# Optimization experiments

Hardware: AMD Instinct MI355X
Metric: run time of the kernel (lower is better)

Reference implementation:

```python
import jax, jax.numpy as jnp
import numpy as np

IN_FEA = 128
OUT_FEA = 128
ALPHA = 0.2  # LeakyReLU negative slope
NEG_INF = -1.0e12


def setup_inputs() -> dict:
    key = jax.random.key(0)
    k1, k2, k3, k4 = jax.random.split(key, 4)
    b, n = 8, 2048
    inp = jax.random.normal(k1, (b, n, IN_FEA), dtype=jnp.float32)
    adj = jax.random.randint(k2, (b, n, n), 0, 2, dtype=jnp.int32)
    # xavier_uniform with gain=1.414
    def xavier(k, shape, gain=1.414):
        fan_in, fan_out = shape[0], shape[1]
        limit = gain * np.sqrt(6.0 / (fan_in + fan_out))
        return jax.random.uniform(k, shape, jnp.float32, -limit, limit)
    W = xavier(k3, (IN_FEA, OUT_FEA))
    a = xavier(k4, (2 * OUT_FEA, 1))
    return {"inp": inp, "adj": adj, "W": W, "a": a}


def reference(inp, adj, W, a):
    # h: [b, n, d]
    h = jnp.matmul(inp, W)
    # Original builds [b, n*n, 2d] via repeat/view; equivalently split a into
    # a1 (applied to h_j, the 'chunks' half) and a2 (applied to h_i).
    d = h.shape[-1]
    a1 = a[:d, 0]   # [d]
    a2 = a[d:, 0]   # [d]
    f1 = jnp.einsum('bnd,d->bn', h, a1)  # contributes per-column (j)
    f2 = jnp.einsum('bnd,d->bn', h, a2)  # contributes per-row (i)
    e = jax.nn.leaky_relu(f2[:, :, None] + f1[:, None, :], negative_slope=ALPHA)  # [b, n, n]
    logits = jnp.where(adj > 0, e, NEG_INF)
    attention = jax.nn.softmax(logits, axis=-1)
    out_h = jnp.matmul(attention, h)
    out_h = jax.nn.elu(out_h) + h  # concat=True branch
    return out_h
```

## Files before the change

### kernel.cpp

```cpp
#include <hip/hip_runtime.h>
#include <hip/hip_bf16.h>

typedef __bf16 bf16x8 __attribute__((ext_vector_type(8)));
typedef __bf16 bf16x4 __attribute__((ext_vector_type(4)));
typedef float  f32x4  __attribute__((ext_vector_type(4)));

#define LRELU_ALPHA 0.2f
#define LOG2E 1.44269504088896340736f

__device__ __forceinline__ float lrelu(float x) { return fmaxf(x, LRELU_ALPHA * x); }
__device__ __forceinline__ float fexp2(float x) { return exp2f(x); }

__device__ __forceinline__ void wg_barrier() {
    asm volatile("s_waitcnt lgkmcnt(0)" ::: "memory");
    __builtin_amdgcn_s_barrier();
    asm volatile("" ::: "memory");
}

__global__ __launch_bounds__(128) void gat_prep(
    const float* __restrict__ inp, const float* __restrict__ W,
    const float* __restrict__ a,
    float* __restrict__ h, float* __restrict__ f1, float* __restrict__ f2)
{
    const int r0 = blockIdx.x << 3;
    const int d  = threadIdx.x;
    __shared__ float sIn[8][128];
    __shared__ float sRed[8][4];
    #pragma unroll
    for (int r = 0; r < 8; ++r)
        sIn[r][d] = inp[(size_t)(r0 + r) * 128 + d];
    __syncthreads();

    float acc[8] = {0.f,0.f,0.f,0.f,0.f,0.f,0.f,0.f};
    #pragma unroll 4
    for (int k = 0; k < 128; ++k) {
        float wv = W[k * 128 + d];
        #pragma unroll
        for (int r = 0; r < 8; ++r) acc[r] += sIn[r][k] * wv;
    }

    const float a1 = a[d], a2 = a[128 + d];
    const int wv = d >> 6;
    #pragma unroll
    for (int r = 0; r < 8; ++r) {
        h[(size_t)(r0 + r) * 128 + d] = acc[r];
        float t1 = acc[r] * a1;
        float t2 = acc[r] * a2;
        #pragma unroll
        for (int m = 1; m < 64; m <<= 1) {
            t1 += __shfl_xor(t1, m);
            t2 += __shfl_xor(t2, m);
        }
        if ((d & 63) == 0) { sRed[r][wv] = t1; sRed[r][2 + wv] = t2; }
    }
    __syncthreads();
    if (d < 8) {
        f1[r0 + d] = (sRed[d][0] + sRed[d][1]) * LOG2E;
        f2[r0 + d] = (sRed[d][2] + sRed[d][3]) * LOG2E;
    }
}

__global__ __launch_bounds__(256) void gat_f1max(
    const float* __restrict__ f1, float* __restrict__ f1max)
{
    const int b = blockIdx.x;
    const int t = threadIdx.x;
    float m = -1e30f;
    for (int j = t; j < 2048; j += 256) m = fmaxf(m, f1[b * 2048 + j]);
    #pragma unroll
    for (int k = 1; k < 64; k <<= 1) m = fmaxf(m, __shfl_xor(m, k));
    __shared__ float sm[4];
    if ((t & 63) == 0) sm[t >> 6] = m;
    __syncthreads();
    if (t == 0) f1max[b] = fmaxf(fmaxf(sm[0], sm[1]), fmaxf(sm[2], sm[3]));
}

__global__ __launch_bounds__(256) void gat_transpose(
    const float* __restrict__ h, __bf16* __restrict__ hT)
{
    __shared__ __bf16 tile[64][72];
    const int tid = threadIdx.x;
    const int bidx = blockIdx.x;
    const int b  = bidx >> 6;
    const int tI = bidx & 63;
    const int n0 = (tI >> 1) << 6;
    const int d0 = (tI & 1) << 6;
    #pragma unroll
    for (int pass = 0; pass < 2; ++pass) {
        int row = (tid >> 3) + (pass << 5);
        int c   = (tid & 7) << 3;
        const float* src = h + (size_t)(b * 2048 + n0 + row) * 128 + d0 + c;
        float4 v0 = *(const float4*)src;
        float4 v1 = *(const float4*)(src + 4);
        __bf16* tp = &tile[row][c];
        tp[0]=(__bf16)v0.x; tp[1]=(__bf16)v0.y; tp[2]=(__bf16)v0.z; tp[3]=(__bf16)v0.w;
        tp[4]=(__bf16)v1.x; tp[5]=(__bf16)v1.y; tp[6]=(__bf16)v1.z; tp[7]=(__bf16)v1.w;
    }
    __syncthreads();
    #pragma unroll
    for (int pass = 0; pass < 2; ++pass) {
        int dd = (tid >> 3) + (pass << 5);
        int nn = (tid & 7) << 3;
        union { __bf16 e[8]; bf16x8 v; } u;
        #pragma unroll
        for (int x = 0; x < 8; ++x) u.e[x] = tile[nn + x][dd];
        *(bf16x8*)(hT + ((size_t)(b * 128 + d0 + dd) << 11) + n0 + nn) = u.v;
    }
}

#define SWZH(row, byteoff) ((byteoff) ^ (((row) & 7) << 4))

__global__ __launch_bounds__(512, 4) void gat_attn4(
    const int* __restrict__ adj, const float* __restrict__ h,
    const __bf16* __restrict__ hT, const float* __restrict__ f1g,
    const float* __restrict__ f2g, const float* __restrict__ f1maxg,
    float* __restrict__ out)
{
    const int bid = ((blockIdx.x & 7) << 6) | (blockIdx.x >> 3);
    const int b  = bid >> 6;
    const int i0 = (bid & 63) << 5;
    const int tid = threadIdx.x;

    __shared__ float  f1s[2048];
    __shared__ alignas(16) __bf16 hTs[2][128 * 64];
    __shared__ alignas(16) __bf16 Ps[32 * 64];
    __shared__ float  lsum[32];

    *(float4*)&f1s[tid << 2] = *(const float4*)&f1g[(b << 11) + (tid << 2)];

    const int pi  = tid >> 4;
    const int pj4 = tid & 15;
    const float fm  = f1maxg[b];
    const float f2v = f2g[(b << 11) + i0 + pi];
    const float Mshift = lrelu(f2v + fm) - 1000.0f;
    const int* ajp = adj + (((size_t)(b << 11) + i0 + pi) << 11) + (pj4 << 2);
    __bf16* pw = Ps + (pi << 6) + (SWZH(pi, pj4 << 3) >> 1);

    const int hd0 = tid >> 3;
    const int hjc = (tid & 7) << 3;
    const __bf16* hgp0 = hT + (((size_t)(b << 7) + hd0) << 11) + hjc;
    const __bf16* hgp1 = hT + (((size_t)(b << 7) + hd0 + 64) << 11) + hjc;
    const int hw0 = (hd0 << 6) + (SWZH(hd0, hjc << 1) >> 1);
    const int hw1 = ((hd0 + 64) << 6) + (SWZH(hd0, hjc << 1) >> 1);

    const int w    = tid >> 6;
    const int lane = tid & 63;
    const int il   = lane & 15;
    const int kg   = lane >> 4;
    const int ig   = w & 1;
    const int dq   = w >> 1;
    const int ai   = (ig << 4) + il;
    const int d0r  = (dq << 5) + il;
    const int d1r  = d0r + 16;
    const int aof0 = (ai << 6)  + (SWZH(ai,       kg << 4) >> 1);
    const int aof1 = (ai << 6)  + (SWZH(ai, 64 | (kg << 4)) >> 1);
    const int bof00 = (d0r << 6) + (SWZH(d0r,       kg << 4) >> 1);
    const int bof01 = (d0r << 6) + (SWZH(d0r, 64 | (kg << 4)) >> 1);
    const int bof10 = (d1r << 6) + (SWZH(d1r,       kg << 4) >> 1);
    const int bof11 = (d1r << 6) + (SWZH(d1r, 64 | (kg << 4)) >> 1);

    int4   gA  = *(const int4*)ajp;
    int4   gA2 = *(const int4*)(ajp + 64);
    bf16x8 gH0 = *(const bf16x8*)hgp0;
    bf16x8 gH1 = *(const bf16x8*)hgp1;
    *(bf16x8*)(hTs[0] + hw0) = gH0;
    *(bf16x8*)(hTs[0] + hw1) = gH1;
    gH0 = *(const bf16x8*)(hgp0 + 64);
    gH1 = *(const bf16x8*)(hgp1 + 64);

    f32x4 acc0 = {0.f,0.f,0.f,0.f}, acc1 = {0.f,0.f,0.f,0.f};
    float den = 0.f;

    wg_barrier();

    for (int t = 0; t < 32; ++t) {
        int4 adjv = gA;
        gA  = gA2;
        gA2 = *(const int4*)(ajp + (((t + 2) & 31) << 6));

        __bf16* hb = hTs[(t + 1) & 1];
        *(bf16x8*)(hb + hw0) = gH0;
        *(bf16x8*)(hb + hw1) = gH1;
        gH0 = *(const bf16x8*)(hgp0 + (((t + 2) & 31) << 6));
        gH1 = *(const bf16x8*)(hgp1 + (((t + 2) & 31) << 6));

        float4 fv = *(const float4*)&f1s[(t << 6) + (pj4 << 2)];
        float p0, p1, p2, p3;
        { float x = f2v + fv.x; float e = fmaxf(x, LRELU_ALPHA * x) - Mshift;
          p0 = fexp2(__builtin_fmaf(e, (float)adjv.x, -1000.f)); }
        { float x = f2v + fv.y; float e = fmaxf(x, LRELU_ALPHA * x) - Mshift;
          p1 = fexp2(__builtin_fmaf(e, (float)adjv.y, -1000.f)); }
        { float x = f2v + fv.z; float e = fmaxf(x, LRELU_ALPHA * x) - Mshift;
          p2 = fexp2(__builtin_fmaf(e, (float)adjv.z, -1000.f)); }
        { float x = f2v + fv.w; float e = fmaxf(x, LRELU_ALPHA * x) - Mshift;
          p3 = fexp2(__builtin_fmaf(e, (float)adjv.w, -1000.f)); }
        bf16x4 pb;
        pb[0] = (__bf16)p0; pb[1] = (__bf16)p1;
        pb[2] = (__bf16)p2; pb[3] = (__bf16)p3;
        den += (float)pb[0] + (float)pb[1] + (float)pb[2] + (float)pb[3];
        *(bf16x4*)pw = pb;

        wg_barrier();

        const __bf16* hr = hTs[t & 1];
        bf16x8 A0  = *(const bf16x8*)(Ps + aof0);
        bf16x8 A1  = *(const bf16x8*)(Ps + aof1);
        bf16x8 B00 = *(const bf16x8*)(hr + bof00);
        bf16x8 B01 = *(const bf16x8*)(hr + bof01);
        bf16x8 B10 = *(const bf16x8*)(hr + bof10);
        bf16x8 B11 = *(const bf16x8*)(hr + bof11);
        acc0 = __builtin_amdgcn_mfma_f32_16x16x32_bf16(A0, B00, acc0, 0, 0, 0);
        acc0 = __builtin_amdgcn_mfma_f32_16x16x32_bf16(A1, B01, acc0, 0, 0, 0);
        acc1 = __builtin_amdgcn_mfma_f32_16x16x32_bf16(A0, B10, acc1, 0, 0, 0);
        acc1 = __builtin_amdgcn_mfma_f32_16x16x32_bf16(A1, B11, acc1, 0, 0, 0);

        wg_barrier();
    }

    den += __shfl_xor(den, 1);
    den += __shfl_xor(den, 2);
    den += __shfl_xor(den, 4);
    den += __shfl_xor(den, 8);
    if (pj4 == 0) lsum[pi] = den;
    wg_barrier();

    #pragma unroll
    for (int r = 0; r < 4; ++r) {
        const int   row = (kg << 2) + r;
        const float dn  = lsum[(ig << 4) + row];
        const size_t gbase = (((size_t)(b << 11) + i0 + (ig << 4) + row) << 7)
                             + (dq << 5) + il;
        float v, e;
        v = acc0[r] / dn; e = (v > 0.f) ? v : (__expf(v) - 1.f); out[gbase]      = e + h[gbase];
        v = acc1[r] / dn; e = (v > 0.f) ? v : (__expf(v) - 1.f); out[gbase + 16] = e + h[gbase + 16];
    }
}

extern "C" void kernel_launch(void* const* d_in, const int* in_sizes, int n_in,
                              void* d_out, int out_size, void* d_ws, size_t ws_size,
                              hipStream_t stream)
{
    const float* inp = (const float*)d_in[0];
    const int*   adj = (const int*)d_in[1];
    const float* W   = (const float*)d_in[2];
    const float* a   = (const float*)d_in[3];
    float* out = (float*)d_out;

    char* ws = (char*)d_ws;
    float*  h     = (float*)ws;
    __bf16* hT    = (__bf16*)(ws + 8388608);
    float*  f1    = (float*)(ws + 8388608 + 4194304);
    float*  f2    = (float*)(ws + 8388608 + 4194304 + 65536);
    float*  f1max = (float*)(ws + 8388608 + 4194304 + 131072);

    gat_prep<<<2048, 128, 0, stream>>>(inp, W, a, h, f1, f2);
    gat_f1max<<<8, 256, 0, stream>>>(f1, f1max);
    gat_transpose<<<512, 256, 0, stream>>>(h, hT);
    gat_attn4<<<512, 512, 0, stream>>>(adj, h, hT, f1, f2, f1max, out);
}
```

Before: 61.48 us.

## Pre-pack h into MFMA fragment layout and software-pipeline P computation

The transpose kernel now writes h in bf16, already arranged in the per-lane MFMA B-fragment order. The attention kernel loads B operands straight from global memory into registers and no longer stages them through LDS. The loop is restructured so the probabilities for the next tile are computed while the current tile's MFMAs run, using a double-buffered P tile with one barrier per iteration instead of two. This cuts LDS traffic and synchronisation, but every block now reads the packed h directly from global or L2 memory, and register pressure rises.

```diff
diff --git a/kernel.cpp b/kernel.cpp
--- a/kernel.cpp
+++ b/kernel.cpp
@@ -8,7 +8,6 @@
 #define LRELU_ALPHA 0.2f
 #define LOG2E 1.44269504088896340736f
 
-__device__ __forceinline__ float lrelu(float x) { return fmaxf(x, LRELU_ALPHA * x); }
 __device__ __forceinline__ float fexp2(float x) { return exp2f(x); }
 
 __device__ __forceinline__ void wg_barrier() {
@@ -75,10 +74,10 @@
     if (t == 0) f1max[b] = fmaxf(fmaxf(sm[0], sm[1]), fmaxf(sm[2], sm[3]));
 }
 
-__global__ __launch_bounds__(256) void gat_transpose(
-    const float* __restrict__ h, __bf16* __restrict__ hT)
-{
-    __shared__ __bf16 tile[64][72];
+__global__ __launch_bounds__(256) void gat_pack(
+    const float* __restrict__ h, __bf16* __restrict__ pack)
+{
+    __shared__ __bf16 tile[64][74];
     const int tid = threadIdx.x;
     const int bidx = blockIdx.x;
     const int b  = bidx >> 6;
@@ -97,22 +96,46 @@
         tp[4]=(__bf16)v1.x; tp[5]=(__bf16)v1.y; tp[6]=(__bf16)v1.z; tp[7]=(__bf16)v1.w;
     }
     __syncthreads();
+    const int lane = tid & 63;
+    const int il = lane & 15;
+    const int kg = lane >> 4;
     #pragma unroll
     for (int pass = 0; pass < 2; ++pass) {
-        int dd = (tid >> 3) + (pass << 5);
-        int nn = (tid & 7) << 3;
+        const int f  = (tid >> 6) + (pass << 2);
+        const int Dl = f >> 1;
+        const int jh = f & 1;
         union { __bf16 e[8]; bf16x8 v; } u;
         #pragma unroll
-        for (int x = 0; x < 8; ++x) u.e[x] = tile[nn + x][dd];
-        *(bf16x8*)(hT + ((size_t)(b * 128 + d0 + dd) << 11) + n0 + nn) = u.v;
-    }
-}
-
-#define SWZH(row, byteoff) ((byteoff) ^ (((row) & 7) << 4))
-
-__global__ __launch_bounds__(512, 4) void gat_attn4(
+        for (int e = 0; e < 8; ++e)
+            u.e[e] = tile[(jh << 5) + (kg << 3) + e][(Dl << 4) + il];
+        const size_t off = (((size_t)(b << 5) + (n0 >> 6)) << 13)
+                         + ((size_t)((((d0 >> 4) + Dl) << 1) | jh) << 9)
+                         + (lane << 3);
+        *(bf16x8*)(pack + off) = u.v;
+    }
+}
+
+#define PCOMPUTE(TT, BUF) do {                                                \
+    float4 fv = *(const float4*)&f1s[((TT) << 6) + (pj4 << 2)];               \
+    float p0, p1, p2, p3;                                                     \
+    { float x = f2v + fv.x; float e = fmaxf(x, LRELU_ALPHA * x) - Mshift;     \
+      p0 = fexp2(__builtin_fmaf(e, (float)gA.x, -1000.f)); }                  \
+    { float x = f2v + fv.y; float e = fmaxf(x, LRELU_ALPHA * x) - Mshift;     \
+      p1 = fexp2(__builtin_fmaf(e, (float)gA.y, -1000.f)); }                  \
+    { float x = f2v + fv.z; float e = fmaxf(x, LRELU_ALPHA * x) - Mshift;     \
+      p2 = fexp2(__builtin_fmaf(e, (float)gA.z, -1000.f)); }                  \
+    { float x = f2v + fv.w; float e = fmaxf(x, LRELU_ALPHA * x) - Mshift;     \
+      p3 = fexp2(__builtin_fmaf(e, (float)gA.w, -1000.f)); }                  \
+    bf16x4 pb;                                                                \
+    pb[0] = (__bf16)p0; pb[1] = (__bf16)p1;                                   \
+    pb[2] = (__bf16)p2; pb[3] = (__bf16)p3;                                   \
+    den += (float)pb[0] + (float)pb[1] + (float)pb[2] + (float)pb[3];         \
+    *(bf16x4*)(&Ps[BUF][pwo]) = pb;                                           \
+} while (0)
+
+__global__ __launch_bounds__(512, 4) void gat_attn5(
     const int* __restrict__ adj, const float* __restrict__ h,
-    const __bf16* __restrict__ hT, const float* __restrict__ f1g,
+    const __bf16* __restrict__ pack, const float* __restrict__ f1g,
     const float* __restrict__ f2g, const float* __restrict__ f1maxg,
     float* __restrict__ out)
 {
@@ -121,10 +144,9 @@
     const int i0 = (bid & 63) << 5;
     const int tid = threadIdx.x;
 
-    __shared__ float  f1s[2048];
-    __shared__ alignas(16) __bf16 hTs[2][128 * 64];
-    __shared__ alignas(16) __bf16 Ps[32 * 64];
-    __shared__ float  lsum[32];
+    __shared__ float f1s[2048];
+    __shared__ alignas(16) __bf16 Ps[2][2048];
+    __shared__ float lsum[32];
 
     *(float4*)&f1s[tid << 2] = *(const float4*)&f1g[(b << 11) + (tid << 2)];
 
@@ -132,16 +154,9 @@
     const int pj4 = tid & 15;
     const float fm  = f1maxg[b];
     const float f2v = f2g[(b << 11) + i0 + pi];
-    const float Mshift = lrelu(f2v + fm) - 1000.0f;
+    const float Mshift = fmaxf(f2v + fm, LRELU_ALPHA * (f2v + fm)) - 1000.0f;
     const int* ajp = adj + (((size_t)(b << 11) + i0 + pi) << 11) + (pj4 << 2);
-    __bf16* pw = Ps + (pi << 6) + (SWZH(pi, pj4 << 3) >> 1);
-
-    const int hd0 = tid >> 3;
-    const int hjc = (tid & 7) << 3;
-    const __bf16* hgp0 = hT + (((size_t)(b << 7) + hd0) << 11) + hjc;
-    const __bf16* hgp1 = hT + (((size_t)(b << 7) + hd0 + 64) << 11) + hjc;
-    const int hw0 = (hd0 << 6) + (SWZH(hd0, hjc << 1) >> 1);
-    const int hw1 = ((hd0 + 64) << 6) + (SWZH(hd0, hjc << 1) >> 1);
+    const int pwo = (pi << 6) + ((((pj4 << 3)) ^ ((pi & 7) << 4)) >> 1);
 
     const int w    = tid >> 6;
     const int lane = tid & 63;
@@ -150,71 +165,59 @@
     const int ig   = w & 1;
     const int dq   = w >> 1;
     const int ai   = (ig << 4) + il;
-    const int d0r  = (dq << 5) + il;
-    const int d1r  = d0r + 16;
-    const int aof0 = (ai << 6)  + (SWZH(ai,       kg << 4) >> 1);
-    const int aof1 = (ai << 6)  + (SWZH(ai, 64 | (kg << 4)) >> 1);
-    const int bof00 = (d0r << 6) + (SWZH(d0r,       kg << 4) >> 1);
-    const int bof01 = (d0r << 6) + (SWZH(d0r, 64 | (kg << 4)) >> 1);
-    const int bof10 = (d1r << 6) + (SWZH(d1r,       kg << 4) >> 1);
-    const int bof11 = (d1r << 6) + (SWZH(d1r, 64 | (kg << 4)) >> 1);
-
-    int4   gA  = *(const int4*)ajp;
-    int4   gA2 = *(const int4*)(ajp + 64);
-    bf16x8 gH0 = *(const bf16x8*)hgp0;
-    bf16x8 gH1 = *(const bf16x8*)hgp1;
-    *(bf16x8*)(hTs[0] + hw0) = gH0;
-    *(bf16x8*)(hTs[0] + hw1) = gH1;
-    gH0 = *(const bf16x8*)(hgp0 + 64);
-    gH1 = *(const bf16x8*)(hgp1 + 64);
+    const int aof0 = (ai << 6) + (((kg << 4) ^ ((ai & 7) << 4)) >> 1);
+    const int aof1 = (ai << 6) + (((64 | (kg << 4)) ^ ((ai & 7) << 4)) >> 1);
+    const __bf16* pB = pack + (((size_t)b << 5) << 13) + (dq << 11) + (lane << 3);
 
     f32x4 acc0 = {0.f,0.f,0.f,0.f}, acc1 = {0.f,0.f,0.f,0.f};
     float den = 0.f;
 
+    int4 gA  = *(const int4*)ajp;
+    int4 gA2 = *(const int4*)(ajp + 64);
+    bf16x8 Bc0 = *(const bf16x8*)(pB);
+    bf16x8 Bc1 = *(const bf16x8*)(pB + 512);
+    bf16x8 Bc2 = *(const bf16x8*)(pB + 1024);
+    bf16x8 Bc3 = *(const bf16x8*)(pB + 1536);
+
     wg_barrier();
 
-    for (int t = 0; t < 32; ++t) {
-        int4 adjv = gA;
-        gA  = gA2;
-        gA2 = *(const int4*)(ajp + (((t + 2) & 31) << 6));
-
-        __bf16* hb = hTs[(t + 1) & 1];
-        *(bf16x8*)(hb + hw0) = gH0;
-        *(bf16x8*)(hb + hw1) = gH1;
-        gH0 = *(const bf16x8*)(hgp0 + (((t + 2) & 31) << 6));
-        gH1 = *(const bf16x8*)(hgp1 + (((t + 2) & 31) << 6));
-
-        float4 fv = *(const float4*)&f1s[(t << 6) + (pj4 << 2)];
-        float p0, p1, p2, p3;
-        { float x = f2v + fv.x; float e = fmaxf(x, LRELU_ALPHA * x) - Mshift;
-          p0 = fexp2(__builtin_fmaf(e, (float)adjv.x, -1000.f)); }
-        { float x = f2v + fv.y; float e = fmaxf(x, LRELU_ALPHA * x) - Mshift;
-          p1 = fexp2(__builtin_fmaf(e, (float)adjv.y, -1000.f)); }
-        { float x = f2v + fv.z; float e = fmaxf(x, LRELU_ALPHA * x) - Mshift;
-          p2 = fexp2(__builtin_fmaf(e, (float)adjv.z, -1000.f)); }
-        { float x = f2v + fv.w; float e = fmaxf(x, LRELU_ALPHA * x) - Mshift;
-          p3 = fexp2(__builtin_fmaf(e, (float)adjv.w, -1000.f)); }
-        bf16x4 pb;
-        pb[0] = (__bf16)p0; pb[1] = (__bf16)p1;
-        pb[2] = (__bf16)p2; pb[3] = (__bf16)p3;
-        den += (float)pb[0] + (float)pb[1] + (float)pb[2] + (float)pb[3];
-        *(bf16x4*)pw = pb;
+    PCOMPUTE(0, 0);
+    gA = gA2;
+    gA2 = *(const int4*)(ajp + 128);
+
+    wg_barrier();
+
+    for (int t = 0; t < 31; ++t) {
+        const __bf16* pBn = pB + ((size_t)(t + 1) << 13);
+        bf16x8 Bn0 = *(const bf16x8*)(pBn);
+        bf16x8 Bn1 = *(const bf16x8*)(pBn + 512);
+        bf16x8 Bn2 = *(const bf16x8*)(pBn + 1024);
+        bf16x8 Bn3 = *(const bf16x8*)(pBn + 1536);
+
+        bf16x8 A0 = *(const bf16x8*)(&Ps[t & 1][aof0]);
+        bf16x8 A1 = *(const bf16x8*)(&Ps[t & 1][aof1]);
+
+        PCOMPUTE(t + 1, (t + 1) & 1);
+        gA = gA2;
+        gA2 = *(const int4*)(ajp + (((t + 3) & 31) << 6));
+
+        acc0 = __builtin_amdgcn_mfma_f32_16x16x32_bf16(A0, Bc0, acc0, 0, 0, 0);
+        acc0 = __builtin_amdgcn_mfma_f32_16x16x32_bf16(A1, Bc1, acc0, 0, 0, 0);
+        acc1 = __builtin_amdgcn_mfma_f32_16x16x32_bf16(A0, Bc2, acc1, 0, 0, 0);
+        acc1 = __builtin_amdgcn_mfma_f32_16x16x32_bf16(A1, Bc3, acc1, 0, 0, 0);
+
+        Bc0 = Bn0; Bc1 = Bn1; Bc2 = Bn2; Bc3 = Bn3;
 
         wg_barrier();
-
-        const __bf16* hr = hTs[t & 1];
-        bf16x8 A0  = *(const bf16x8*)(Ps + aof0);
-        bf16x8 A1  = *(const bf16x8*)(Ps + aof1);
-        bf16x8 B00 = *(const bf16x8*)(hr + bof00);
-        bf16x8 B01 = *(const bf16x8*)(hr + bof01);
-        bf16x8 B10 = *(const bf16x8*)(hr + bof10);
-        bf16x8 B11 = *(const bf16x8*)(hr + bof11);
-        acc0 = __builtin_amdgcn_mfma_f32_16x16x32_bf16(A0, B00, acc0, 0, 0, 0);
-        acc0 = __builtin_amdgcn_mfma_f32_16x16x32_bf16(A1, B01, acc0, 0, 0, 0);
-        acc1 = __builtin_amdgcn_mfma_f32_16x16x32_bf16(A0, B10, acc1, 0, 0, 0);
-        acc1 = __builtin_amdgcn_mfma_f32_16x16x32_bf16(A1, B11, acc1, 0, 0, 0);
-
-        wg_barrier();
+    }
+
+    {
+        bf16x8 A0 = *(const bf16x8*)(&Ps[1][aof0]);
+        bf16x8 A1 = *(const bf16x8*)(&Ps[1][aof1]);
+        acc0 = __builtin_amdgcn_mfma_f32_16x16x32_bf16(A0, Bc0, acc0, 0, 0, 0);
+        acc0 = __builtin_amdgcn_mfma_f32_16x16x32_bf16(A1, Bc1, acc0, 0, 0, 0);
+        acc1 = __builtin_amdgcn_mfma_f32_16x16x32_bf16(A0, Bc2, acc1, 0, 0, 0);
+        acc1 = __builtin_amdgcn_mfma_f32_16x16x32_bf16(A1, Bc3, acc1, 0, 0, 0);
     }
 
     den += __shfl_xor(den, 1);
@@ -248,13 +251,13 @@
 
     char* ws = (char*)d_ws;
     float*  h     = (float*)ws;
-    __bf16* hT    = (__bf16*)(ws + 8388608);
+    __bf16* pack  = (__bf16*)(ws + 8388608);
     float*  f1    = (float*)(ws + 8388608 + 4194304);
     float*  f2    = (float*)(ws + 8388608 + 4194304 + 65536);
     float*  f1max = (float*)(ws + 8388608 + 4194304 + 131072);
 
     gat_prep<<<2048, 128, 0, stream>>>(inp, W, a, h, f1, f2);
     gat_f1max<<<8, 256, 0, stream>>>(f1, f1max);
-    gat_transpose<<<512, 256, 0, stream>>>(h, hT);
-    gat_attn4<<<512, 512, 0, stream>>>(adj, h, hT, f1, f2, f1max, out);
-}
+    gat_pack<<<512, 256, 0, stream>>>(h, pack);
+    gat_attn5<<<512, 512, 0, stream>>>(adj, h, pack, f1, f2, f1max, out);
+}
```

After: 59.60 us. 3.1% less time.
